# Performance work log

Measured on AMD Instinct MI355X. Metric: run time of the kernel, lower is better.

The kernel has to match this reference:

```python
import jax, jax.numpy as jnp
import numpy as np

N = 50000
NFEAT, NHID, NCLASS, HEADS = 256, 64, 40, 4
HEAD_DIM = NHID // HEADS
E = 800000
NEG_SLOPE = 0.2


def _gat_conv(x, src, dst, W, a_src, a_dst, b, heads):
    # x: [N, F_in], W: [F_in, heads*C], a_src/a_dst: [heads, C], b: [heads*C]
    n = x.shape[0]
    h = (x @ W).reshape(n, heads, -1)                      # [N, H, C]
    alpha_s = jnp.einsum('nhc,hc->nh', h, a_src)           # [N, H]
    alpha_d = jnp.einsum('nhc,hc->nh', h, a_dst)
    e = jax.nn.leaky_relu(alpha_s[src] + alpha_d[dst], NEG_SLOPE)  # [E, H]
    # scatter-softmax over incoming edges per destination node
    e_max = jax.ops.segment_max(e, dst, num_segments=n)
    e_exp = jnp.exp(e - e_max[dst])
    denom = jax.ops.segment_sum(e_exp, dst, num_segments=n)
    alpha = e_exp / (denom[dst] + 1e-16)                   # [E, H]
    msg = h[src] * alpha[:, :, None]                       # [E, H, C]
    out = jax.ops.segment_sum(msg, dst, num_segments=n)    # [N, H, C]
    return out.reshape(n, -1) + b


def setup_inputs() -> dict:
    key = jax.random.key(0)
    ks = jax.random.split(key, 16)
    x = jax.random.normal(ks[0], (N, NFEAT), dtype=jnp.float32)
    edge_index = jax.random.randint(ks[1], (2, E), 0, N, dtype=jnp.int64)

    def glorot(k, shape):
        fan = sum(shape[:2]) if len(shape) > 1 else shape[0]
        return jax.random.normal(k, shape, dtype=jnp.float32) * (1.0 / np.sqrt(fan))

    inp = {'x': x, 'edge_index': edge_index}
    # conv1: nfeat -> heads*head_dim
    inp['W1'] = glorot(ks[2], (NFEAT, HEADS * HEAD_DIM))
    inp['a_src1'] = glorot(ks[3], (HEADS, HEAD_DIM))
    inp['a_dst1'] = glorot(ks[4], (HEADS, HEAD_DIM))
    inp['b1'] = jnp.zeros((HEADS * HEAD_DIM,), dtype=jnp.float32)
    # convx[0]: nhid -> heads*head_dim
    inp['W2'] = glorot(ks[5], (NHID, HEADS * HEAD_DIM))
    inp['a_src2'] = glorot(ks[6], (HEADS, HEAD_DIM))
    inp['a_dst2'] = glorot(ks[7], (HEADS, HEAD_DIM))
    inp['b2'] = jnp.zeros((HEADS * HEAD_DIM,), dtype=jnp.float32)
    # conv2: nhid -> nclass, heads=1
    inp['W3'] = glorot(ks[8], (NHID, NCLASS))
    inp['a_src3'] = glorot(ks[9], (1, NCLASS))
    inp['a_dst3'] = glorot(ks[10], (1, NCLASS))
    inp['b3'] = jnp.zeros((NCLASS,), dtype=jnp.float32)
    return inp


def reference(x, edge_index, W1, a_src1, a_dst1, b1, W2, a_src2, a_dst2, b2, W3, a_src3, a_dst3, b3):
    # add self-loops (PyG GATConv default add_self_loops=True)
    loop = jnp.arange(N, dtype=edge_index.dtype)
    src = jnp.concatenate([edge_index[0], loop])
    dst = jnp.concatenate([edge_index[1], loop])

    h = jax.nn.relu(_gat_conv(x, src, dst, W1, a_src1, a_dst1, b1, HEADS))
    h = jax.nn.relu(_gat_conv(h, src, dst, W2, a_src2, a_dst2, b2, HEADS))
    out = _gat_conv(h, src, dst, W3, a_src3, a_dst3, b3, 1)
    return out
```

## Files before the change

### kernel.cpp

```cpp
#include <hip/hip_runtime.h>

#define NEG_SLOPE 0.2f
#define SCAN_CHUNK 2048


__global__ void init_hist(int* __restrict__ hist, int n) {
    int i = blockIdx.x * blockDim.x + threadIdx.x;
    if (i < n) hist[i] = 1;
}

__global__ __launch_bounds__(256) void edge_hist(const int* __restrict__ ei,
                                                 int* __restrict__ hist,
                                                 int E, float inv8) {
    const int part = blockIdx.x & 7;
    const int base = (blockIdx.x >> 3) * 2048;
    const int end  = min(base + 2048, E);
    for (int i = base + (int)threadIdx.x; i < end; i += 256) {
        int d = ei[E + i];
        int pd = min((int)((float)d * inv8), 7);
        if (pd == part) atomicAdd(&hist[d], 1);
    }
}


__global__ __launch_bounds__(256) void scan_partial(const int* __restrict__ hist,
                                                    int* __restrict__ bsum, int n) {
    const int base = blockIdx.x * SCAN_CHUNK;
    const int tid = threadIdx.x;
    int s = 0;
    #pragma unroll
    for (int i = 0; i < 8; ++i) {
        int idx = base + tid * 8 + i;
        if (idx < n) s += hist[idx];
    }
    #pragma unroll
    for (int d = 1; d < 64; d <<= 1) s += __shfl_xor(s, d);
    __shared__ int wsum[4];
    if ((tid & 63) == 0) wsum[tid >> 6] = s;
    __syncthreads();
    if (tid == 0) bsum[blockIdx.x] = wsum[0] + wsum[1] + wsum[2] + wsum[3];
}

__global__ void scan_bsums(const int* __restrict__ bsum, int* __restrict__ boff,
                           int nb, int* __restrict__ rowptr, int n) {
    const int tid = threadIdx.x;
    int v = (tid < nb) ? bsum[tid] : 0;
    int sv = v;
    #pragma unroll
    for (int d = 1; d < 64; d <<= 1) {
        int t = __shfl_up(sv, d);
        if (tid >= d) sv += t;
    }
    if (tid < nb) boff[tid] = sv - v;
    if (tid == 63) rowptr[n] = sv;
}

__global__ __launch_bounds__(256) void scan_final(const int* __restrict__ hist,
                                                  const int* __restrict__ boff,
                                                  int* __restrict__ rowptr,
                                                  int* __restrict__ fill, int n) {
    const int base = blockIdx.x * SCAN_CHUNK;
    const int tid = threadIdx.x;
    const int lane = tid & 63, wv = tid >> 6;
    int vals[8];
    int s = 0;
    #pragma unroll
    for (int i = 0; i < 8; ++i) {
        int idx = base + tid * 8 + i;
        vals[i] = (idx < n) ? hist[idx] : 0;
        s += vals[i];
    }
    int sv = s;
    #pragma unroll
    for (int d = 1; d < 64; d <<= 1) {
        int t = __shfl_up(sv, d);
        if (lane >= d) sv += t;
    }
    __shared__ int wsum[4];
    if (lane == 63) wsum[wv] = sv;
    __syncthreads();
    int woff = 0;
    for (int i = 0; i < wv; ++i) woff += wsum[i];
    int excl = boff[blockIdx.x] + woff + sv - s;
    #pragma unroll
    for (int i = 0; i < 8; ++i) {
        int idx = base + tid * 8 + i;
        if (idx < n) { rowptr[idx] = excl; fill[idx] = excl; }
        excl += vals[i];
    }
}

__global__ __launch_bounds__(256) void scatter_part(const int* __restrict__ ei,
                                                    int* __restrict__ fill,
                                                    int* __restrict__ col,
                                                    int E, int M, float inv8) {
    const int part = blockIdx.x & 7;
    const int base = (blockIdx.x >> 3) * 2048;
    const int end  = min(base + 2048, M);
    for (int i = base + (int)threadIdx.x; i < end; i += 256) {
        int d = (i < E) ? ei[E + i] : (i - E);
        int pd = min((int)((float)d * inv8), 7);
        if (pd != part) continue;
        int s = (i < E) ? ei[i] : d;
        int pos = atomicAdd(&fill[d], 1);
        col[pos] = s;
    }
}


template <int K, int HC, int AH>
__global__ __launch_bounds__(256) void gemm_tiled(
    const float* __restrict__ x, const float* __restrict__ W,
    const float* __restrict__ a_src, const float* __restrict__ a_dst,
    float* __restrict__ h, float* __restrict__ as_, float* __restrict__ ad_,
    int n) {
    __shared__ float xs[64][68];
    __shared__ float ws[64][64];
    const int t = threadIdx.x;
    const int tx = t & 15;
    const int ty = t >> 4;
    const int rowBase = blockIdx.x * 64;

    float acc[4][4];
    #pragma unroll
    for (int r = 0; r < 4; ++r)
        #pragma unroll
        for (int c = 0; c < 4; ++c) acc[r][c] = 0.f;

    const int sr = t >> 2;
    const int sq = t & 3;

    #pragma unroll 1
    for (int kb = 0; kb < K; kb += 64) {
        __syncthreads();
        {
            int g = rowBase + sr;
            const float* xr = x + (size_t)g * K + kb;
            #pragma unroll
            for (int i = 0; i < 4; ++i) {
                int ko = sq * 16 + i * 4;
                float4 v = make_float4(0.f, 0.f, 0.f, 0.f);
                if (g < n) v = *(const float4*)(xr + ko);
                *(float4*)&xs[sr][ko] = v;
            }
        }
        if (HC == 64) {
            #pragma unroll
            for (int i = 0; i < 4; ++i) {
                int li = t + i * 256;
                int k = li >> 4, j4 = (li & 15) * 4;
                *(float4*)&ws[k][j4] = *(const float4*)&W[(size_t)(kb + k) * 64 + j4];
            }
        } else {
            for (int i = t; i < 64 * 64; i += 256) {
                int k = i >> 6, j = i & 63;
                ws[k][j] = (j < HC) ? W[(size_t)(kb + k) * HC + j] : 0.f;
            }
        }
        __syncthreads();

        #pragma unroll 2
        for (int k = 0; k < 64; k += 4) {
            float xr[4][4];
            #pragma unroll
            for (int r = 0; r < 4; ++r) {
                float4 v = *(const float4*)&xs[ty * 4 + r][k];
                xr[r][0] = v.x; xr[r][1] = v.y; xr[r][2] = v.z; xr[r][3] = v.w;
            }
            float wr[4][4];
            #pragma unroll
            for (int kk = 0; kk < 4; ++kk) {
                float4 v = *(const float4*)&ws[k + kk][tx * 4];
                wr[kk][0] = v.x; wr[kk][1] = v.y; wr[kk][2] = v.z; wr[kk][3] = v.w;
            }
            #pragma unroll
            for (int kk = 0; kk < 4; ++kk)
                #pragma unroll
                for (int r = 0; r < 4; ++r)
                    #pragma unroll
                    for (int c = 0; c < 4; ++c)
                        acc[r][c] = fmaf(xr[r][kk], wr[kk][c], acc[r][c]);
        }
    }

    if (AH == 4) {
        const int hh = tx >> 2;
        const int cb = (tx & 3) * 4;
        float asv[4], adv[4];
        #pragma unroll
        for (int c = 0; c < 4; ++c) {
            asv[c] = a_src[hh * 16 + cb + c];
            adv[c] = a_dst[hh * 16 + cb + c];
        }
        #pragma unroll
        for (int r = 0; r < 4; ++r) {
            float ps = 0.f, pd = 0.f;
            #pragma unroll
            for (int c = 0; c < 4; ++c) {
                ps = fmaf(acc[r][c], asv[c], ps);
                pd = fmaf(acc[r][c], adv[c], pd);
            }
            ps += __shfl_xor(ps, 1); ps += __shfl_xor(ps, 2);
            pd += __shfl_xor(pd, 1); pd += __shfl_xor(pd, 2);
            int g = rowBase + ty * 4 + r;
            if (g < n) {
                float4 v = make_float4(acc[r][0], acc[r][1], acc[r][2], acc[r][3]);
                *(float4*)&h[(size_t)g * 64 + tx * 4] = v;
                if ((tx & 3) == 0) {
                    as_[g * 4 + hh] = ps;
                    ad_[g * 4 + hh] = pd;
                }
            }
        }
    } else if (AH == 1) {
        const int cb = tx * 4;
        float asv[4], adv[4];
        #pragma unroll
        for (int c = 0; c < 4; ++c) {
            bool vld = (cb + c) < HC;
            asv[c] = vld ? a_src[cb + c] : 0.f;
            adv[c] = vld ? a_dst[cb + c] : 0.f;
        }
        #pragma unroll
        for (int r = 0; r < 4; ++r) {
            float ps = 0.f, pd = 0.f;
            #pragma unroll
            for (int c = 0; c < 4; ++c) {
                ps = fmaf(acc[r][c], asv[c], ps);
                pd = fmaf(acc[r][c], adv[c], pd);
            }
            ps += __shfl_xor(ps, 1); ps += __shfl_xor(ps, 2);
            ps += __shfl_xor(ps, 4); ps += __shfl_xor(ps, 8);
            pd += __shfl_xor(pd, 1); pd += __shfl_xor(pd, 2);
            pd += __shfl_xor(pd, 4); pd += __shfl_xor(pd, 8);
            int g = rowBase + ty * 4 + r;
            if (g < n) {
                if (tx * 4 < HC) {
                    float4 v = make_float4(acc[r][0], acc[r][1], acc[r][2], acc[r][3]);
                    *(float4*)&h[(size_t)g * HC + tx * 4] = v;
                }
                if (tx == 0) { as_[g] = ps; ad_[g] = pd; }
            }
        }
    } else {
        #pragma unroll
        for (int r = 0; r < 4; ++r) {
            int g = rowBase + ty * 4 + r;
            if (g < n && tx * 4 < HC) {
                float4 v = make_float4(acc[r][0], acc[r][1], acc[r][2], acc[r][3]);
                *(float4*)&h[(size_t)g * HC + tx * 4] = v;
            }
        }
    }
}

template <int H, int C, bool RELU>
__global__ __launch_bounds__(256) void aggr_kernel(
    const float* __restrict__ h, const float* __restrict__ as_,
    const float* __restrict__ ad_, const int* __restrict__ rowptr,
    const int* __restrict__ col, const float* __restrict__ b,
    float* __restrict__ out, int n) {
    constexpr int HC = H * C;
    __shared__ float wls[4][64][H];
    __shared__ int   sls[4][64];
    const int wib  = threadIdx.x >> 6;
    const int lane = threadIdx.x & 63;
    const int wid  = blockIdx.x * 4 + wib;
    if (wid >= n) return;

    const int p0 = rowptr[wid], p1 = rowptr[wid + 1];
    const int deg = p1 - p0;

    float adv[H];
    #pragma unroll
    for (int hh = 0; hh < H; ++hh) adv[hh] = ad_[wid * H + hh];

    const int myh = (HC < 64 && lane >= HC) ? 0 : lane / C;

    float m[H], sum[H];
    #pragma unroll
    for (int hh = 0; hh < H; ++hh) { m[hh] = -3.4e38f; sum[hh] = 0.f; }
    float acc = 0.f;

    for (int ch = 0; ch * 64 < deg; ++ch) {
        const int idx = p0 + ch * 64 + lane;
        const bool valid = idx < p1;
        int s = 0;
        float e[H];
        if (valid) {
            s = col[idx];
            if (H == 4) {
                float4 a4 = *(const float4*)&as_[s * 4];
                e[0] = a4.x + adv[0]; e[1] = a4.y + adv[1];
                e[2] = a4.z + adv[2]; e[3] = a4.w + adv[3];
            } else {
                e[0] = as_[s] + adv[0];
            }
            #pragma unroll
            for (int hh = 0; hh < H; ++hh)
                e[hh] = (e[hh] >= 0.f) ? e[hh] : NEG_SLOPE * e[hh];
        } else {
            #pragma unroll
            for (int hh = 0; hh < H; ++hh) e[hh] = -3.4e38f;
        }
        float f[H], w[H];
        #pragma unroll
        for (int hh = 0; hh < H; ++hh) {
            float v = e[hh];
            #pragma unroll
            for (int d = 1; d < 64; d <<= 1) v = fmaxf(v, __shfl_xor(v, d));
            float mn = fmaxf(m[hh], v);
            f[hh] = expf(m[hh] - mn);
            m[hh] = mn;
            w[hh] = expf(e[hh] - mn);
        }
        #pragma unroll
        for (int hh = 0; hh < H; ++hh) {
            float v = w[hh];
            #pragma unroll
            for (int d = 1; d < 64; d <<= 1) v += __shfl_xor(v, d);
            sum[hh] = sum[hh] * f[hh] + v;
        }
        #pragma unroll
        for (int hh = 0; hh < H; ++hh) wls[wib][lane][hh] = w[hh];
        sls[wib][lane] = s;
        __builtin_amdgcn_wave_barrier();

        float fmy;
        if (H == 1) fmy = f[0];
        else {
            float a = (myh & 1) ? f[1] : f[0];
            float c2 = (myh & 1) ? f[3] : f[2];
            fmy = (myh & 2) ? c2 : a;
        }
        acc *= fmy;

        const int cnt = min(64, deg - ch * 64);
        int p = 0;
        for (; p + 4 <= cnt; p += 4) {
            int s0 = sls[wib][p],     s1 = sls[wib][p + 1];
            int s2 = sls[wib][p + 2], s3 = sls[wib][p + 3];
            float w0 = wls[wib][p][myh],     w1 = wls[wib][p + 1][myh];
            float w2 = wls[wib][p + 2][myh], w3 = wls[wib][p + 3][myh];
            float h0 = 0.f, h1 = 0.f, h2 = 0.f, h3 = 0.f;
            if (lane < HC) {
                h0 = h[(size_t)s0 * HC + lane];
                h1 = h[(size_t)s1 * HC + lane];
                h2 = h[(size_t)s2 * HC + lane];
                h3 = h[(size_t)s3 * HC + lane];
            }
            acc = fmaf(w0, h0, acc);
            acc = fmaf(w1, h1, acc);
            acc = fmaf(w2, h2, acc);
            acc = fmaf(w3, h3, acc);
        }
        for (; p < cnt; ++p) {
            int ss = sls[wib][p];
            float ww = wls[wib][p][myh];
            float hv = (lane < HC) ? h[(size_t)ss * HC + lane] : 0.f;
            acc = fmaf(ww, hv, acc);
        }
        __builtin_amdgcn_wave_barrier();
    }

    if (lane < HC) {
        float smy;
        if (H == 1) smy = sum[0];
        else {
            float a = (myh & 1) ? sum[1] : sum[0];
            float c2 = (myh & 1) ? sum[3] : sum[2];
            smy = (myh & 2) ? c2 : a;
        }
        float r = acc / (smy + 1e-16f) + b[lane];
        out[(size_t)wid * HC + lane] = RELU ? fmaxf(r, 0.f) : r;
    }
}


extern "C" void kernel_launch(void* const* d_in, const int* in_sizes, int n_in,
                              void* d_out, int out_size, void* d_ws, size_t ws_size,
                              hipStream_t stream) {
    const float* x      = (const float*)d_in[0];
    const int*   ei     = (const int*)d_in[1];
    const float* W1     = (const float*)d_in[2];
    const float* a_src1 = (const float*)d_in[3];
    const float* a_dst1 = (const float*)d_in[4];
    const float* b1     = (const float*)d_in[5];
    const float* W2     = (const float*)d_in[6];
    const float* a_src2 = (const float*)d_in[7];
    const float* a_dst2 = (const float*)d_in[8];
    const float* b2     = (const float*)d_in[9];
    const float* W3     = (const float*)d_in[10];
    const float* a_src3 = (const float*)d_in[11];
    const float* a_dst3 = (const float*)d_in[12];
    const float* b3     = (const float*)d_in[13];
    float* out = (float*)d_out;

    const int NFEAT = 256, NHID = 64;
    const int N = in_sizes[0] / NFEAT;
    const int E = in_sizes[1] / 2;
    const int M = E + N;
    const float inv8 = 8.0f / (float)N;
    const int nb = (N + SCAN_CHUNK - 1) / SCAN_CHUNK;

    char* p = (char*)d_ws;
    auto alloc = [&](size_t bytes) {
        char* r = p;
        p += (bytes + 255) & ~(size_t)255;
        return r;
    };
    int*   hist   = (int*)alloc((size_t)N * 4);
    int*   rowptr = (int*)alloc((size_t)(N + 1) * 4);
    int*   fill   = (int*)alloc((size_t)N * 4);
    int*   col    = (int*)alloc((size_t)M * 4);
    float* hbuf   = (float*)alloc((size_t)N * NHID * 4);
    float* xbuf   = (float*)alloc((size_t)N * NHID * 4);
    float* asb    = (float*)alloc((size_t)N * 4 * 4);
    float* adb    = (float*)alloc((size_t)N * 4 * 4);
    int*   bsum   = (int*)alloc((size_t)64 * 4);
    int*   boff   = (int*)alloc((size_t)64 * 4);

    dim3 blk(256);
    const int gemmGrid = (N + 63) / 64;
    const int aggrGrid = (N + 3) / 4;

    init_hist<<<(N + 255) / 256, blk, 0, stream>>>(hist, N);
    edge_hist<<<8 * ((E + 2047) / 2048), blk, 0, stream>>>(ei, hist, E, inv8);
    scan_partial<<<nb, blk, 0, stream>>>(hist, bsum, N);
    scan_bsums<<<1, 64, 0, stream>>>(bsum, boff, nb, rowptr, N);
    scan_final<<<nb, blk, 0, stream>>>(hist, boff, rowptr, fill, N);
    scatter_part<<<8 * ((M + 2047) / 2048), blk, 0, stream>>>(ei, fill, col, E, M, inv8);

    gemm_tiled<256, 64, 4><<<gemmGrid, blk, 0, stream>>>(
        x, W1, a_src1, a_dst1, hbuf, asb, adb, N);
    aggr_kernel<4, 16, true><<<aggrGrid, blk, 0, stream>>>(
        hbuf, asb, adb, rowptr, col, b1, xbuf, N);

    gemm_tiled<64, 64, 4><<<gemmGrid, blk, 0, stream>>>(
        xbuf, W2, a_src2, a_dst2, hbuf, asb, adb, N);
    aggr_kernel<4, 16, true><<<aggrGrid, blk, 0, stream>>>(
        hbuf, asb, adb, rowptr, col, b2, xbuf, N);

    gemm_tiled<64, 40, 1><<<gemmGrid, blk, 0, stream>>>(
        xbuf, W3, a_src3, a_dst3, hbuf, asb, adb, N);
    aggr_kernel<1, 40, false><<<aggrGrid, blk, 0, stream>>>(
        hbuf, asb, adb, rowptr, col, b3, out, N);
}
```

Measured before the change: 374.2 us.

## Drop max-subtraction in GAT softmax and split edges across half-waves with float2 loads

The aggregation kernel no longer does the online max and rescaling for the softmax. It computes exp of the leaky-relu logits directly with fast __expf and accumulates the denominator alongside the weighted sum, which removes two 64-wide shuffle reductions per head per chunk. Each wave now splits into two halves that handle alternating edges, each lane loading a float2 of features, and the halves are combined with one cross-half shuffle at the end. This relies on the logits being small enough that exp does not overflow, so it is less robust numerically than the max-subtracted form.

```diff
diff --git a/kernel.cpp b/kernel.cpp
--- a/kernel.cpp
+++ b/kernel.cpp
@@ -261,8 +261,9 @@
     const int* __restrict__ col, const float* __restrict__ b,
     float* __restrict__ out, int n) {
     constexpr int HC = H * C;
-    __shared__ float wls[4][64][H];
-    __shared__ int   sls[4][64];
+    constexpr int HC2 = HC / 2;
+    __shared__ __align__(16) float wls[4][64][H];
+    __shared__ int sls[4][64];
     const int wib  = threadIdx.x >> 6;
     const int lane = threadIdx.x & 63;
     const int wid  = blockIdx.x * 4 + wib;
@@ -275,20 +276,22 @@
     #pragma unroll
     for (int hh = 0; hh < H; ++hh) adv[hh] = ad_[wid * H + hh];
 
-    const int myh = (HC < 64 && lane >= HC) ? 0 : lane / C;
-
-    float m[H], sum[H];
-    #pragma unroll
-    for (int hh = 0; hh < H; ++hh) { m[hh] = -3.4e38f; sum[hh] = 0.f; }
-    float acc = 0.f;
+    const int half = lane >> 5;
+    const int sl   = lane & 31;
+    const int myh2 = (2 * sl) / C;
+    const bool act = (2 * sl) < HC;
+
+    float2 acc = make_float2(0.f, 0.f);
+    float sumw = 0.f;
 
     for (int ch = 0; ch * 64 < deg; ++ch) {
         const int idx = p0 + ch * 64 + lane;
         const bool valid = idx < p1;
         int s = 0;
-        float e[H];
+        float w[H];
         if (valid) {
             s = col[idx];
+            float e[H];
             if (H == 4) {
                 float4 a4 = *(const float4*)&as_[s * 4];
                 e[0] = a4.x + adv[0]; e[1] = a4.y + adv[1];
@@ -297,82 +300,52 @@
                 e[0] = as_[s] + adv[0];
             }
             #pragma unroll
-            for (int hh = 0; hh < H; ++hh)
-                e[hh] = (e[hh] >= 0.f) ? e[hh] : NEG_SLOPE * e[hh];
+            for (int hh = 0; hh < H; ++hh) {
+                float ee = (e[hh] >= 0.f) ? e[hh] : NEG_SLOPE * e[hh];
+                w[hh] = __expf(ee);
+            }
         } else {
             #pragma unroll
-            for (int hh = 0; hh < H; ++hh) e[hh] = -3.4e38f;
-        }
-        float f[H], w[H];
-        #pragma unroll
-        for (int hh = 0; hh < H; ++hh) {
-            float v = e[hh];
-            #pragma unroll
-            for (int d = 1; d < 64; d <<= 1) v = fmaxf(v, __shfl_xor(v, d));
-            float mn = fmaxf(m[hh], v);
-            f[hh] = expf(m[hh] - mn);
-            m[hh] = mn;
-            w[hh] = expf(e[hh] - mn);
-        }
-        #pragma unroll
-        for (int hh = 0; hh < H; ++hh) {
-            float v = w[hh];
-            #pragma unroll
-            for (int d = 1; d < 64; d <<= 1) v += __shfl_xor(v, d);
-            sum[hh] = sum[hh] * f[hh] + v;
-        }
-        #pragma unroll
-        for (int hh = 0; hh < H; ++hh) wls[wib][lane][hh] = w[hh];
+            for (int hh = 0; hh < H; ++hh) w[hh] = 0.f;
+        }
+        if (H == 4) {
+            *(float4*)&wls[wib][lane][0] = make_float4(w[0], w[1], w[2], w[3]);
+        } else {
+            wls[wib][lane][0] = w[0];
+        }
         sls[wib][lane] = s;
         __builtin_amdgcn_wave_barrier();
 
-        float fmy;
-        if (H == 1) fmy = f[0];
-        else {
-            float a = (myh & 1) ? f[1] : f[0];
-            float c2 = (myh & 1) ? f[3] : f[2];
-            fmy = (myh & 2) ? c2 : a;
-        }
-        acc *= fmy;
-
         const int cnt = min(64, deg - ch * 64);
-        int p = 0;
-        for (; p + 4 <= cnt; p += 4) {
-            int s0 = sls[wib][p],     s1 = sls[wib][p + 1];
-            int s2 = sls[wib][p + 2], s3 = sls[wib][p + 3];
-            float w0 = wls[wib][p][myh],     w1 = wls[wib][p + 1][myh];
-            float w2 = wls[wib][p + 2][myh], w3 = wls[wib][p + 3][myh];
-            float h0 = 0.f, h1 = 0.f, h2 = 0.f, h3 = 0.f;
-            if (lane < HC) {
-                h0 = h[(size_t)s0 * HC + lane];
-                h1 = h[(size_t)s1 * HC + lane];
-                h2 = h[(size_t)s2 * HC + lane];
-                h3 = h[(size_t)s3 * HC + lane];
-            }
-            acc = fmaf(w0, h0, acc);
-            acc = fmaf(w1, h1, acc);
-            acc = fmaf(w2, h2, acc);
-            acc = fmaf(w3, h3, acc);
-        }
-        for (; p < cnt; ++p) {
-            int ss = sls[wib][p];
-            float ww = wls[wib][p][myh];
-            float hv = (lane < HC) ? h[(size_t)ss * HC + lane] : 0.f;
-            acc = fmaf(ww, hv, acc);
+        #pragma unroll 2
+        for (int p = 0; p < cnt; p += 2) {
+            const int pi = p + half;
+            float ww = 0.f;
+            int ss = 0;
+            if (pi < cnt) {
+                ww = wls[wib][pi][myh2];
+                ss = sls[wib][pi];
+            }
+            float2 hv = make_float2(0.f, 0.f);
+            if (act && pi < cnt)
+                hv = *(const float2*)&h[(size_t)ss * HC + 2 * sl];
+            acc.x = fmaf(ww, hv.x, acc.x);
+            acc.y = fmaf(ww, hv.y, acc.y);
+            sumw += ww;
         }
         __builtin_amdgcn_wave_barrier();
     }
 
-    if (lane < HC) {
-        float smy;
-        if (H == 1) smy = sum[0];
-        else {
-            float a = (myh & 1) ? sum[1] : sum[0];
-            float c2 = (myh & 1) ? sum[3] : sum[2];
-            smy = (myh & 2) ? c2 : a;
-        }
-        float r = acc / (smy + 1e-16f) + b[lane];
-        out[(size_t)wid * HC + lane] = RELU ? fmaxf(r, 0.f) : r;
+    acc.x += __shfl_xor(acc.x, 32);
+    acc.y += __shfl_xor(acc.y, 32);
+    sumw  += __shfl_xor(sumw, 32);
+
+    if (half == 0 && act) {
+        float inv = 1.f / (sumw + 1e-16f);
+        float r0 = acc.x * inv + b[2 * sl];
+        float r1 = acc.y * inv + b[2 * sl + 1];
+        if (RELU) { r0 = fmaxf(r0, 0.f); r1 = fmaxf(r1, 0.f); }
+        *(float2*)&out[(size_t)wid * HC + 2 * sl] = make_float2(r0, r1);
     }
 }
 
```

Measured after the change: 362.4 us. 1.03x faster.
